# Optimization experiments

Measured on AMD Instinct MI355X. Metric: run time of the kernel, lower is better.

## Reference

```python
import jax, jax.numpy as jnp
import numpy as np
import math

B, S, H, D = 4, 4096, 2048, 128  # batch, seq_len, hidden_dim, head_size

def setup_inputs() -> dict:
    key = jax.random.key(0)
    ks = jax.random.split(key, 7)
    scale = 1.0 / math.sqrt(H)
    return {
        "x": jax.random.normal(ks[0], (B, S, H), dtype=jnp.float32),
        "Wq": jax.random.normal(ks[1], (H, D), dtype=jnp.float32) * scale,
        "bq": jnp.zeros((D,), dtype=jnp.float32),
        "Wk": jax.random.normal(ks[2], (H, D), dtype=jnp.float32) * scale,
        "bk": jnp.zeros((D,), dtype=jnp.float32),
        "Wv": jax.random.normal(ks[3], (H, D), dtype=jnp.float32) * scale,
        "bv": jnp.zeros((D,), dtype=jnp.float32),
    }

def reference(x, Wq, bq, Wk, bk, Wv, bv):
    # projections: [B,S,D]
    q = x @ Wq + bq
    k = x @ Wk + bk
    v = x @ Wv + bv
    # raw scores [B,S,S] with causal mask, NO pre-softmax scaling (as in source)
    scores = jnp.einsum('bsd,btd->bst', q, k)
    causal = jnp.tril(jnp.ones((S, S), dtype=bool))
    scores = jnp.where(causal, scores, -jnp.inf)
    # non-standard: scale AFTER softmax by 1/sqrt(head_size)
    w = jax.nn.softmax(scores, axis=-1) * (1.0 / math.sqrt(D))
    # dropout p=0.0 -> identity
    return jnp.einsum('bst,btd->bsd', w, v)
```

## Files before the change

### kernel.cpp

```cpp
#include <hip/hip_runtime.h>
#include <math.h>
#include <stdint.h>

#define SEQ   4096
#define HID   2048
#define HD    128
#define NROWS 16384

typedef __attribute__((ext_vector_type(8))) short bf16x8;
typedef __attribute__((ext_vector_type(4))) float f32x4;

static constexpr float OSCALE = 0.088388347648318447f;

using gvptr = const __attribute__((address_space(1))) void*;
using lvptr = __attribute__((address_space(3))) void*;
__device__ __forceinline__ void gld_lds16(const void* g, void* l) {
    __builtin_amdgcn_global_load_lds((gvptr)g, (lvptr)l, 16, 0, 0);
}

__device__ __forceinline__ unsigned short f2bf_rne(float f) {
    union { float f; unsigned u; } v; v.f = f;
    unsigned u = v.u + 0x7fffu + ((v.u >> 16) & 1u);
    return (unsigned short)(u >> 16);
}
__device__ __forceinline__ unsigned short f2bf_tr(float f) {
    union { float f; unsigned u; } v; v.f = f;
    return (unsigned short)(v.u >> 16);
}
__device__ __forceinline__ float bf2f(unsigned short h) {
    union { unsigned u; float f; } v; v.u = ((unsigned)h) << 16;
    return v.f;
}

__global__ __launch_bounds__(256) void prep_w(
    const float* __restrict__ Wq, const float* __restrict__ Wk, const float* __restrict__ Wv,
    unsigned short* __restrict__ wth, unsigned short* __restrict__ wtl)
{
    __shared__ float T[64][68];
    const int tid = threadIdx.x;
    const int k0 = blockIdx.x * 64, n0 = blockIdx.y * 64, mm = blockIdx.z;
    const float* W = (mm == 0) ? Wq : (mm == 1) ? Wk : Wv;
    #pragma unroll
    for (int i = 0; i < 4; ++i) {
        const int fi = i * 256 + tid, kk = fi >> 4, nc = (fi & 15) * 4;
        const float4 w = *(const float4*)(W + (size_t)(k0 + kk) * HD + n0 + nc);
        T[kk][nc] = w.x; T[kk][nc + 1] = w.y; T[kk][nc + 2] = w.z; T[kk][nc + 3] = w.w;
    }
    __syncthreads();
    unsigned short* oh = wth + (size_t)mm * HD * HID;
    unsigned short* ol = wtl + (size_t)mm * HD * HID;
    #pragma unroll
    for (int i = 0; i < 4; ++i) {
        const int fi = i * 256 + tid, nn = fi >> 4, kc = (fi & 15) * 4;
        const float a = T[kc][nn], b = T[kc + 1][nn], c = T[kc + 2][nn], d = T[kc + 3][nn];
        ushort4 hv, lv;
        hv.x = f2bf_rne(a); hv.y = f2bf_rne(b); hv.z = f2bf_rne(c); hv.w = f2bf_rne(d);
        lv.x = f2bf_rne(a - bf2f(hv.x)); lv.y = f2bf_rne(b - bf2f(hv.y));
        lv.z = f2bf_rne(c - bf2f(hv.z)); lv.w = f2bf_rne(d - bf2f(hv.w));
        *(ushort4*)(oh + (size_t)(n0 + nn) * HID + k0 + kc) = hv;
        *(ushort4*)(ol + (size_t)(n0 + nn) * HID + k0 + kc) = lv;
    }
}

__global__ __launch_bounds__(256, 3) void qkv_fused(
    const float* __restrict__ x,
    const float* __restrict__ bq, const float* __restrict__ bk, const float* __restrict__ bv,
    const unsigned short* __restrict__ wth, const unsigned short* __restrict__ wtl,
    unsigned short* __restrict__ qh, unsigned short* __restrict__ ql,
    unsigned short* __restrict__ kh, unsigned short* __restrict__ kl,
    unsigned short* __restrict__ vth)
{
    __shared__ unsigned short Ah[64][40], Al[64][40];
    __shared__ unsigned short Bt[5][64][32];

    const int tid = threadIdx.x, wave = tid >> 6, lane = tid & 63;
    const int l15 = lane & 15, q4 = lane >> 4;
    const int wr = wave >> 1, wc = wave & 1;
    const int r0 = (blockIdx.x >> 1) * 64;
    const int hc = blockIdx.x & 1;

    const unsigned short* wsrc0 = wth + (size_t)hc * 64 * HID;
    const unsigned short* wsrc1 = wtl + (size_t)hc * 64 * HID;
    const unsigned short* wsrc2 = wth + (size_t)HD * HID + (size_t)hc * 64 * HID;
    const unsigned short* wsrc3 = wtl + (size_t)HD * HID + (size_t)hc * 64 * HID;
    const unsigned short* wsrc4 = wth + (size_t)2 * HD * HID + (size_t)hc * 64 * HID;

    const int srow = wave * 16 + (lane >> 2);
    const int schunk = ((lane & 3) ^ ((lane >> 2) & 3)) * 8;
    const int pchunk = (q4 ^ (l15 & 3)) * 8;
    const int bro = wc * 32;

    f32x4 accq[2][2], acck[2][2], accv[2][2];
    #pragma unroll
    for (int i = 0; i < 2; ++i)
        #pragma unroll
        for (int j = 0; j < 2; ++j) {
            accq[i][j] = (f32x4){0.f, 0.f, 0.f, 0.f};
            acck[i][j] = (f32x4){0.f, 0.f, 0.f, 0.f};
            accv[i][j] = (f32x4){0.f, 0.f, 0.f, 0.f};
        }

    for (int k0 = 0; k0 < HID; k0 += 32) {
        float4 xv[2];
        #pragma unroll
        for (int i = 0; i < 2; ++i) {
            const int fi = i * 256 + tid, row = fi >> 3, kc = (fi & 7) * 4;
            xv[i] = *(const float4*)(x + (size_t)(r0 + row) * HID + k0 + kc);
        }
        __syncthreads();
        {
            gld_lds16(wsrc0 + (size_t)srow * HID + k0 + schunk, &Bt[0][wave * 16][0]);
            gld_lds16(wsrc1 + (size_t)srow * HID + k0 + schunk, &Bt[1][wave * 16][0]);
            gld_lds16(wsrc2 + (size_t)srow * HID + k0 + schunk, &Bt[2][wave * 16][0]);
            gld_lds16(wsrc3 + (size_t)srow * HID + k0 + schunk, &Bt[3][wave * 16][0]);
            gld_lds16(wsrc4 + (size_t)srow * HID + k0 + schunk, &Bt[4][wave * 16][0]);
        }
        #pragma unroll
        for (int i = 0; i < 2; ++i) {
            const int fi = i * 256 + tid, row = fi >> 3, kc = (fi & 7) * 4;
            ushort4 hv, lv;
            hv.x = f2bf_tr(xv[i].x); hv.y = f2bf_tr(xv[i].y);
            hv.z = f2bf_tr(xv[i].z); hv.w = f2bf_tr(xv[i].w);
            lv.x = f2bf_tr(xv[i].x - bf2f(hv.x)); lv.y = f2bf_tr(xv[i].y - bf2f(hv.y));
            lv.z = f2bf_tr(xv[i].z - bf2f(hv.z)); lv.w = f2bf_tr(xv[i].w - bf2f(hv.w));
            *(ushort4*)&Ah[row][kc] = hv;
            *(ushort4*)&Al[row][kc] = lv;
        }
        __syncthreads();

        bf16x8 ah[2], al[2];
        #pragma unroll
        for (int mt = 0; mt < 2; ++mt) {
            ah[mt] = *(const bf16x8*)&Ah[wr * 32 + mt * 16 + l15][q4 * 8];
            al[mt] = *(const bf16x8*)&Al[wr * 32 + mt * 16 + l15][q4 * 8];
        }
        #pragma unroll
        for (int nt = 0; nt < 2; ++nt) {
            const int br = bro + nt * 16 + l15;
            const bf16x8 qbh = *(const bf16x8*)&Bt[0][br][pchunk];
            const bf16x8 qbl = *(const bf16x8*)&Bt[1][br][pchunk];
            #pragma unroll
            for (int mt = 0; mt < 2; ++mt) {
                accq[mt][nt] = __builtin_amdgcn_mfma_f32_16x16x32_bf16(ah[mt], qbh, accq[mt][nt], 0, 0, 0);
                accq[mt][nt] = __builtin_amdgcn_mfma_f32_16x16x32_bf16(ah[mt], qbl, accq[mt][nt], 0, 0, 0);
                accq[mt][nt] = __builtin_amdgcn_mfma_f32_16x16x32_bf16(al[mt], qbh, accq[mt][nt], 0, 0, 0);
            }
            const bf16x8 kbh = *(const bf16x8*)&Bt[2][br][pchunk];
            const bf16x8 kbl = *(const bf16x8*)&Bt[3][br][pchunk];
            #pragma unroll
            for (int mt = 0; mt < 2; ++mt) {
                acck[mt][nt] = __builtin_amdgcn_mfma_f32_16x16x32_bf16(ah[mt], kbh, acck[mt][nt], 0, 0, 0);
                acck[mt][nt] = __builtin_amdgcn_mfma_f32_16x16x32_bf16(ah[mt], kbl, acck[mt][nt], 0, 0, 0);
                acck[mt][nt] = __builtin_amdgcn_mfma_f32_16x16x32_bf16(al[mt], kbh, acck[mt][nt], 0, 0, 0);
            }
            const bf16x8 vbh = *(const bf16x8*)&Bt[4][br][pchunk];
            #pragma unroll
            for (int mt = 0; mt < 2; ++mt)
                accv[mt][nt] = __builtin_amdgcn_mfma_f32_16x16x32_bf16(ah[mt], vbh, accv[mt][nt], 0, 0, 0);
        }
    }

    #pragma unroll
    for (int nt = 0; nt < 2; ++nt) {
        const int col = hc * 64 + wc * 32 + nt * 16 + l15;
        const float bbq = bq[col], bbk = bk[col], bbv = bv[col];
        #pragma unroll
        for (int mt = 0; mt < 2; ++mt) {
            const int Rb = r0 + wr * 32 + mt * 16 + q4 * 4;
            #pragma unroll
            for (int r = 0; r < 4; ++r) {
                const float vq = accq[mt][nt][r] + bbq;
                const unsigned short hq = f2bf_rne(vq);
                qh[(size_t)(Rb + r) * HD + col] = hq;
                ql[(size_t)(Rb + r) * HD + col] = f2bf_rne(vq - bf2f(hq));
                const float vk = acck[mt][nt][r] + bbk;
                const unsigned short hk = f2bf_rne(vk);
                kh[(size_t)(Rb + r) * HD + col] = hk;
                kl[(size_t)(Rb + r) * HD + col] = f2bf_rne(vk - bf2f(hk));
            }
            const int bi = Rb >> 12, s0 = Rb & 4095;
            ushort4 pv;
            pv.x = f2bf_rne(accv[mt][nt][0] + bbv);
            pv.y = f2bf_rne(accv[mt][nt][1] + bbv);
            pv.z = f2bf_rne(accv[mt][nt][2] + bbv);
            pv.w = f2bf_rne(accv[mt][nt][3] + bbv);
            *(ushort4*)(vth + ((size_t)(bi * HD + col)) * SEQ + s0) = pv;
        }
    }
}

__global__ __launch_bounds__(256, 2) void flash_mfma(
    const unsigned short* __restrict__ qh, const unsigned short* __restrict__ ql,
    const unsigned short* __restrict__ kh, const unsigned short* __restrict__ kl,
    const unsigned short* __restrict__ vth,
    unsigned short* __restrict__ oPb, float* __restrict__ mP, float* __restrict__ lP)
{
    __shared__ unsigned short Kh[64][128], Kl[64][128];
    __shared__ unsigned short Vt[128][64];
    __shared__ unsigned short Ps[4][16][72];

    const int tid = threadIdx.x, wave = tid >> 6, lane = tid & 63;
    const int l15 = lane & 15, q4 = lane >> 4;
    const int h = blockIdx.x & 3, pair = (blockIdx.x >> 2) & 31, b = blockIdx.x >> 7;

    const int krow_l = lane >> 4;
    const int vrow_l = lane >> 3;
    const int vsc = ((lane & 7) ^ (vrow_l & 7)) * 8;
    const int kkey7 = l15 & 7;
    const int vkey7 = l15 & 7;

    for (int side = 0; side < 2; ++side) {
        const int tt = side ? (63 - pair) : pair;
        const int n = tt + 1;
        const int j0 = (n * h) >> 2, j1 = (n * (h + 1)) >> 2;

        const int qrow = b * SEQ + tt * 64 + wave * 16 + l15;
        bf16x8 aqh[4], aql[4];
        #pragma unroll
        for (int ks = 0; ks < 4; ++ks) {
            aqh[ks] = *(const bf16x8*)(qh + (size_t)qrow * HD + ks * 32 + q4 * 8);
            aql[ks] = *(const bf16x8*)(ql + (size_t)qrow * HD + ks * 32 + q4 * 8);
        }
        f32x4 oa[8];
        #pragma unroll
        for (int d = 0; d < 8; ++d) oa[d] = (f32x4){0.f, 0.f, 0.f, 0.f};
        float m_r[4] = {-INFINITY, -INFINITY, -INFINITY, -INFINITY};
        float l_r[4] = {0.f, 0.f, 0.f, 0.f};

        for (int j = j0; j < j1; ++j) {
            __syncthreads();
            {
                const size_t kb = (size_t)b * SEQ + j * 64;
                #pragma unroll
                for (int c = 0; c < 4; ++c) {
                    const int rl = c * 4 + krow_l;
                    const int sc = (l15 ^ (rl & 7)) * 8;
                    const size_t gr = (kb + wave * 16 + rl) * HD + sc;
                    gld_lds16(kh + gr, &Kh[wave * 16 + c * 4][0]);
                    gld_lds16(kl + gr, &Kl[wave * 16 + c * 4][0]);
                }
                #pragma unroll
                for (int c = 0; c < 4; ++c)
                    gld_lds16(vth + ((size_t)(b * HD + wave * 32 + c * 8 + vrow_l)) * SEQ
                                  + j * 64 + vsc,
                              &Vt[wave * 32 + c * 8][0]);
            }
            __syncthreads();

            f32x4 s[4];
            #pragma unroll
            for (int nt = 0; nt < 4; ++nt) s[nt] = (f32x4){0.f, 0.f, 0.f, 0.f};
            #pragma unroll
            for (int ks = 0; ks < 4; ++ks) {
                const int pc = ((ks * 4 + q4) ^ kkey7) * 8;
                #pragma unroll
                for (int nt = 0; nt < 4; ++nt) {
                    const bf16x8 bh = *(const bf16x8*)&Kh[nt * 16 + l15][pc];
                    const bf16x8 bl = *(const bf16x8*)&Kl[nt * 16 + l15][pc];
                    s[nt] = __builtin_amdgcn_mfma_f32_16x16x32_bf16(aqh[ks], bh, s[nt], 0, 0, 0);
                    s[nt] = __builtin_amdgcn_mfma_f32_16x16x32_bf16(aql[ks], bh, s[nt], 0, 0, 0);
                    s[nt] = __builtin_amdgcn_mfma_f32_16x16x32_bf16(aqh[ks], bl, s[nt], 0, 0, 0);
                }
            }
            if (j == tt) {
                #pragma unroll
                for (int nt = 0; nt < 4; ++nt) {
                    const int cl = nt * 16 + l15;
                    #pragma unroll
                    for (int r = 0; r < 4; ++r) {
                        const int rl = wave * 16 + q4 * 4 + r;
                        if (cl > rl) s[nt][r] = -INFINITY;
                    }
                }
            }
            #pragma unroll
            for (int r = 0; r < 4; ++r) {
                float mt = fmaxf(fmaxf(s[0][r], s[1][r]), fmaxf(s[2][r], s[3][r]));
                mt = fmaxf(mt, __shfl_xor(mt, 1));
                mt = fmaxf(mt, __shfl_xor(mt, 2));
                mt = fmaxf(mt, __shfl_xor(mt, 4));
                mt = fmaxf(mt, __shfl_xor(mt, 8));
                const float mn = fmaxf(m_r[r], mt);
                const float al = __expf(m_r[r] - mn);
                m_r[r] = mn;
                const float p0 = __expf(s[0][r] - mn), p1 = __expf(s[1][r] - mn);
                const float p2 = __expf(s[2][r] - mn), p3 = __expf(s[3][r] - mn);
                Ps[wave][q4 * 4 + r][l15]      = f2bf_tr(p0);
                Ps[wave][q4 * 4 + r][16 + l15] = f2bf_tr(p1);
                Ps[wave][q4 * 4 + r][32 + l15] = f2bf_tr(p2);
                Ps[wave][q4 * 4 + r][48 + l15] = f2bf_tr(p3);
                float ps = p0 + p1 + p2 + p3;
                ps += __shfl_xor(ps, 1); ps += __shfl_xor(ps, 2);
                ps += __shfl_xor(ps, 4); ps += __shfl_xor(ps, 8);
                l_r[r] = l_r[r] * al + ps;
                #pragma unroll
                for (int d = 0; d < 8; ++d) oa[d][r] *= al;
            }
            const bf16x8 ap0 = *(const bf16x8*)&Ps[wave][l15][q4 * 8];
            const bf16x8 ap1 = *(const bf16x8*)&Ps[wave][l15][32 + q4 * 8];
            #pragma unroll
            for (int d = 0; d < 8; ++d) {
                const bf16x8 bv0 = *(const bf16x8*)&Vt[d * 16 + l15][(q4 ^ vkey7) * 8];
                const bf16x8 bv1 = *(const bf16x8*)&Vt[d * 16 + l15][((4 + q4) ^ vkey7) * 8];
                oa[d] = __builtin_amdgcn_mfma_f32_16x16x32_bf16(ap0, bv0, oa[d], 0, 0, 0);
                oa[d] = __builtin_amdgcn_mfma_f32_16x16x32_bf16(ap1, bv1, oa[d], 0, 0, 0);
            }
        }

        const int R0 = b * SEQ + tt * 64 + wave * 16 + q4 * 4;
        unsigned short* op = oPb + (size_t)h * NROWS * HD;
        #pragma unroll
        for (int d = 0; d < 8; ++d)
            #pragma unroll
            for (int r = 0; r < 4; ++r)
                op[(size_t)(R0 + r) * HD + d * 16 + l15] = f2bf_rne(oa[d][r]);
        if (l15 == 0) {
            #pragma unroll
            for (int r = 0; r < 4; ++r) {
                mP[h * NROWS + R0 + r] = m_r[r];
                lP[h * NROWS + R0 + r] = l_r[r];
            }
        }
    }
}

__global__ __launch_bounds__(256) void flash_merge(
    const unsigned short* __restrict__ oPb, const float* __restrict__ mP,
    const float* __restrict__ lP, float* __restrict__ out)
{
    const int idx = blockIdx.x * 256 + threadIdx.x;
    const int r = idx >> 5, c = (idx & 31) * 4;
    float m[4], l[4];
    #pragma unroll
    for (int i = 0; i < 4; ++i) { m[i] = mP[i * NROWS + r]; l[i] = lP[i * NROWS + r]; }
    float M = fmaxf(fmaxf(m[0], m[1]), fmaxf(m[2], m[3]));
    float a[4], lsum = 0.f;
    #pragma unroll
    for (int i = 0; i < 4; ++i) { a[i] = __expf(m[i] - M); lsum += l[i] * a[i]; }
    const float inv = OSCALE / lsum;
    float ox = 0.f, oy = 0.f, oz = 0.f, ow = 0.f;
    #pragma unroll
    for (int i = 0; i < 4; ++i) {
        const ushort4 ov = *(const ushort4*)(oPb + (size_t)i * NROWS * HD + (size_t)r * HD + c);
        ox += a[i] * bf2f(ov.x); oy += a[i] * bf2f(ov.y);
        oz += a[i] * bf2f(ov.z); ow += a[i] * bf2f(ov.w);
    }
    float4 o; o.x = ox * inv; o.y = oy * inv; o.z = oz * inv; o.w = ow * inv;
    *(float4*)(out + (size_t)r * HD + c) = o;
}

extern "C" void kernel_launch(void* const* d_in, const int* in_sizes, int n_in,
                              void* d_out, int out_size, void* d_ws, size_t ws_size,
                              hipStream_t stream)
{
    (void)in_sizes; (void)n_in; (void)out_size; (void)ws_size;
    const float* x  = (const float*)d_in[0];
    const float* Wq = (const float*)d_in[1];
    const float* bq = (const float*)d_in[2];
    const float* Wk = (const float*)d_in[3];
    const float* bk = (const float*)d_in[4];
    const float* Wv = (const float*)d_in[5];
    const float* bv = (const float*)d_in[6];
    float* out = (float*)d_out;

    char* w = (char*)d_ws;
    unsigned short* qh  = (unsigned short*)(w);
    unsigned short* ql  = (unsigned short*)(w + 4194304);
    unsigned short* kh  = (unsigned short*)(w + 8388608);
    unsigned short* kl  = (unsigned short*)(w + 12582912);
    unsigned short* vth = (unsigned short*)(w + 16777216);
    unsigned short* wth = (unsigned short*)(w + 20971520);
    unsigned short* wtl = (unsigned short*)(w + 22544384);
    unsigned short* oPb = (unsigned short*)(w + 24117248);
    float* mP = (float*)(w + 40894464);
    float* lP = (float*)(w + 41156608);

    prep_w<<<dim3(32, 2, 3), 256, 0, stream>>>(Wq, Wk, Wv, wth, wtl);
    qkv_fused<<<512, 256, 0, stream>>>(x, bq, bk, bv, wth, wtl, qh, ql, kh, kl, vth);
    flash_mfma<<<512, 256, 0, stream>>>(qh, ql, kh, kl, vth, oPb, mP, lP);
    flash_merge<<<2048, 256, 0, stream>>>(oPb, mP, lP, out);
}
```

Before: 334.5 us.

## Double K-step to 64 and prefetch next x tile into registers in QKV GEMM

The QKV projection kernel now processes 64 columns of the hidden dimension per iteration instead of 32, using larger LDS tiles with an 8-way XOR swizzle for the weight tiles. It also loads the next x tile into registers before the MFMA work of the current one, so global load latency overlaps compute. This halves the number of barriers and loop iterations. In exchange it uses more LDS and registers, and launch bounds drop to 2 blocks per CU, which lowers occupancy.

```diff
diff --git a/kernel.cpp b/kernel.cpp
--- a/kernel.cpp
+++ b/kernel.cpp
@@ -62,7 +62,7 @@
     }
 }
 
-__global__ __launch_bounds__(256, 3) void qkv_fused(
+__global__ __launch_bounds__(256, 2) void qkv_fused(
     const float* __restrict__ x,
     const float* __restrict__ bq, const float* __restrict__ bk, const float* __restrict__ bv,
     const unsigned short* __restrict__ wth, const unsigned short* __restrict__ wtl,
@@ -70,8 +70,8 @@
     unsigned short* __restrict__ kh, unsigned short* __restrict__ kl,
     unsigned short* __restrict__ vth)
 {
-    __shared__ unsigned short Ah[64][40], Al[64][40];
-    __shared__ unsigned short Bt[5][64][32];
+    __shared__ unsigned short Ah[64][72], Al[64][72];
+    __shared__ unsigned short Bt[5][64][64];
 
     const int tid = threadIdx.x, wave = tid >> 6, lane = tid & 63;
     const int l15 = lane & 15, q4 = lane >> 4;
@@ -79,16 +79,15 @@
     const int r0 = (blockIdx.x >> 1) * 64;
     const int hc = blockIdx.x & 1;
 
-    const unsigned short* wsrc0 = wth + (size_t)hc * 64 * HID;
-    const unsigned short* wsrc1 = wtl + (size_t)hc * 64 * HID;
-    const unsigned short* wsrc2 = wth + (size_t)HD * HID + (size_t)hc * 64 * HID;
-    const unsigned short* wsrc3 = wtl + (size_t)HD * HID + (size_t)hc * 64 * HID;
-    const unsigned short* wsrc4 = wth + (size_t)2 * HD * HID + (size_t)hc * 64 * HID;
-
-    const int srow = wave * 16 + (lane >> 2);
-    const int schunk = ((lane & 3) ^ ((lane >> 2) & 3)) * 8;
-    const int pchunk = (q4 ^ (l15 & 3)) * 8;
-    const int bro = wc * 32;
+    const unsigned short* wsrc[5] = {
+        wth + (size_t)hc * 64 * HID,
+        wtl + (size_t)hc * 64 * HID,
+        wth + (size_t)HD * HID + (size_t)hc * 64 * HID,
+        wtl + (size_t)HD * HID + (size_t)hc * 64 * HID,
+        wth + (size_t)2 * HD * HID + (size_t)hc * 64 * HID };
+
+    const int srow_off = lane >> 3;
+    const int schunk   = ((lane & 7) ^ (lane >> 3)) * 8;
 
     f32x4 accq[2][2], acck[2][2], accv[2][2];
     #pragma unroll
@@ -100,24 +99,31 @@
             accv[i][j] = (f32x4){0.f, 0.f, 0.f, 0.f};
         }
 
-    for (int k0 = 0; k0 < HID; k0 += 32) {
-        float4 xv[2];
-        #pragma unroll
-        for (int i = 0; i < 2; ++i) {
-            const int fi = i * 256 + tid, row = fi >> 3, kc = (fi & 7) * 4;
-            xv[i] = *(const float4*)(x + (size_t)(r0 + row) * HID + k0 + kc);
-        }
+    const float* xbase = x + (size_t)r0 * HID;
+
+    float4 xv[4];
+    #pragma unroll
+    for (int i = 0; i < 4; ++i) {
+        const int fi = i * 256 + tid, row = fi >> 4, kc = (fi & 15) * 4;
+        xv[i] = *(const float4*)(xbase + (size_t)row * HID + kc);
+    }
+
+    for (int k0 = 0; k0 < HID; k0 += 64) {
         __syncthreads();
         {
-            gld_lds16(wsrc0 + (size_t)srow * HID + k0 + schunk, &Bt[0][wave * 16][0]);
-            gld_lds16(wsrc1 + (size_t)srow * HID + k0 + schunk, &Bt[1][wave * 16][0]);
-            gld_lds16(wsrc2 + (size_t)srow * HID + k0 + schunk, &Bt[2][wave * 16][0]);
-            gld_lds16(wsrc3 + (size_t)srow * HID + k0 + schunk, &Bt[3][wave * 16][0]);
-            gld_lds16(wsrc4 + (size_t)srow * HID + k0 + schunk, &Bt[4][wave * 16][0]);
-        }
-        #pragma unroll
-        for (int i = 0; i < 2; ++i) {
-            const int fi = i * 256 + tid, row = fi >> 3, kc = (fi & 7) * 4;
+            #pragma unroll
+            for (int a = 0; a < 5; ++a) {
+                #pragma unroll
+                for (int c = 0; c < 2; ++c) {
+                    const int row = wave * 16 + c * 8 + srow_off;
+                    gld_lds16(wsrc[a] + (size_t)row * HID + k0 + schunk,
+                              &Bt[a][wave * 16 + c * 8][0]);
+                }
+            }
+        }
+        #pragma unroll
+        for (int i = 0; i < 4; ++i) {
+            const int fi = i * 256 + tid, row = fi >> 4, kc = (fi & 15) * 4;
             ushort4 hv, lv;
             hv.x = f2bf_tr(xv[i].x); hv.y = f2bf_tr(xv[i].y);
             hv.z = f2bf_tr(xv[i].z); hv.w = f2bf_tr(xv[i].w);
@@ -128,35 +134,46 @@
         }
         __syncthreads();
 
-        bf16x8 ah[2], al[2];
-        #pragma unroll
-        for (int mt = 0; mt < 2; ++mt) {
-            ah[mt] = *(const bf16x8*)&Ah[wr * 32 + mt * 16 + l15][q4 * 8];
-            al[mt] = *(const bf16x8*)&Al[wr * 32 + mt * 16 + l15][q4 * 8];
-        }
-        #pragma unroll
-        for (int nt = 0; nt < 2; ++nt) {
-            const int br = bro + nt * 16 + l15;
-            const bf16x8 qbh = *(const bf16x8*)&Bt[0][br][pchunk];
-            const bf16x8 qbl = *(const bf16x8*)&Bt[1][br][pchunk];
+        const int kn = (k0 + 64 < HID) ? (k0 + 64) : 0;
+        #pragma unroll
+        for (int i = 0; i < 4; ++i) {
+            const int fi = i * 256 + tid, row = fi >> 4, kc = (fi & 15) * 4;
+            xv[i] = *(const float4*)(xbase + (size_t)row * HID + kn + kc);
+        }
+
+        #pragma unroll
+        for (int ks = 0; ks < 2; ++ks) {
+            bf16x8 ah[2], al[2];
             #pragma unroll
             for (int mt = 0; mt < 2; ++mt) {
-                accq[mt][nt] = __builtin_amdgcn_mfma_f32_16x16x32_bf16(ah[mt], qbh, accq[mt][nt], 0, 0, 0);
-                accq[mt][nt] = __builtin_amdgcn_mfma_f32_16x16x32_bf16(ah[mt], qbl, accq[mt][nt], 0, 0, 0);
-                accq[mt][nt] = __builtin_amdgcn_mfma_f32_16x16x32_bf16(al[mt], qbh, accq[mt][nt], 0, 0, 0);
-            }
-            const bf16x8 kbh = *(const bf16x8*)&Bt[2][br][pchunk];
-            const bf16x8 kbl = *(const bf16x8*)&Bt[3][br][pchunk];
-            #pragma unroll
-            for (int mt = 0; mt < 2; ++mt) {
-                acck[mt][nt] = __builtin_amdgcn_mfma_f32_16x16x32_bf16(ah[mt], kbh, acck[mt][nt], 0, 0, 0);
-                acck[mt][nt] = __builtin_amdgcn_mfma_f32_16x16x32_bf16(ah[mt], kbl, acck[mt][nt], 0, 0, 0);
-                acck[mt][nt] = __builtin_amdgcn_mfma_f32_16x16x32_bf16(al[mt], kbh, acck[mt][nt], 0, 0, 0);
-            }
-            const bf16x8 vbh = *(const bf16x8*)&Bt[4][br][pchunk];
-            #pragma unroll
-            for (int mt = 0; mt < 2; ++mt)
-                accv[mt][nt] = __builtin_amdgcn_mfma_f32_16x16x32_bf16(ah[mt], vbh, accv[mt][nt], 0, 0, 0);
+                ah[mt] = *(const bf16x8*)&Ah[wr * 32 + mt * 16 + l15][ks * 32 + q4 * 8];
+                al[mt] = *(const bf16x8*)&Al[wr * 32 + mt * 16 + l15][ks * 32 + q4 * 8];
+            }
+            const int pc = ((ks * 4 + q4) ^ (l15 & 7)) * 8;
+            #pragma unroll
+            for (int nt = 0; nt < 2; ++nt) {
+                const int br = wc * 32 + nt * 16 + l15;
+                const bf16x8 qbh = *(const bf16x8*)&Bt[0][br][pc];
+                const bf16x8 qbl = *(const bf16x8*)&Bt[1][br][pc];
+                #pragma unroll
+                for (int mt = 0; mt < 2; ++mt) {
+                    accq[mt][nt] = __builtin_amdgcn_mfma_f32_16x16x32_bf16(ah[mt], qbh, accq[mt][nt], 0, 0, 0);
+                    accq[mt][nt] = __builtin_amdgcn_mfma_f32_16x16x32_bf16(ah[mt], qbl, accq[mt][nt], 0, 0, 0);
+                    accq[mt][nt] = __builtin_amdgcn_mfma_f32_16x16x32_bf16(al[mt], qbh, accq[mt][nt], 0, 0, 0);
+                }
+                const bf16x8 kbh = *(const bf16x8*)&Bt[2][br][pc];
+                const bf16x8 kbl = *(const bf16x8*)&Bt[3][br][pc];
+                #pragma unroll
+                for (int mt = 0; mt < 2; ++mt) {
+                    acck[mt][nt] = __builtin_amdgcn_mfma_f32_16x16x32_bf16(ah[mt], kbh, acck[mt][nt], 0, 0, 0);
+                    acck[mt][nt] = __builtin_amdgcn_mfma_f32_16x16x32_bf16(ah[mt], kbl, acck[mt][nt], 0, 0, 0);
+                    acck[mt][nt] = __builtin_amdgcn_mfma_f32_16x16x32_bf16(al[mt], kbh, acck[mt][nt], 0, 0, 0);
+                }
+                const bf16x8 vbh = *(const bf16x8*)&Bt[4][br][pc];
+                #pragma unroll
+                for (int mt = 0; mt < 2; ++mt)
+                    accv[mt][nt] = __builtin_amdgcn_mfma_f32_16x16x32_bf16(ah[mt], vbh, accv[mt][nt], 0, 0, 0);
+            }
         }
     }
 
```

Result: faster. 320.1 us (-4.3%).
